# Kernel optimization log

Measured on AMD Instinct MI355X. Metric: run time of the kernel, lower is better.

The kernel has to match this reference:

```python
import jax, jax.numpy as jnp
import numpy as np

N_NODES = 200000
DEG = 16
T = 3


def _w(key, shape, scale=0.05):
    return (jax.random.normal(key, shape, dtype=jnp.float32) * scale)


def setup_inputs() -> dict:
    key = jax.random.key(0)
    ks = jax.random.split(key, 24)
    inp = {
        'h': jax.random.normal(ks[0], (N_NODES, 70), dtype=jnp.float32),
        'edge_feats': jax.random.normal(ks[1], (N_NODES, DEG, 6), dtype=jnp.float32),
        'nbr_idx': jax.random.randint(ks[2], (N_NODES, DEG), 0, N_NODES, dtype=jnp.int32),
        # V: Linear(70,70) (shared across all T rounds, since ModuleList([m]*T) aliases)
        'Vw': _w(ks[3], (70, 70)), 'Vb': _w(ks[4], (70,)),
        # E: Linear(6,6)
        'Ew': _w(ks[5], (6, 6)), 'Eb': _w(ks[6], (6,)),
        # U: Linear(146,70) (shared across rounds)
        'Uw': _w(ks[7], (146, 70)), 'Ub': _w(ks[8], (70,)),
        # R: Linear(140,128)
        'Rw': _w(ks[9], (140, 128)), 'Rb': _w(ks[10], (128,)),
        # shared_hidden1: 128->128, shared_hidden2: 128->100
        'S1w': _w(ks[11], (128, 128)), 'S1b': _w(ks[12], (128,)),
        'S2w': _w(ks[13], (128, 100)), 'S2b': _w(ks[14], (100,)),
        # task head (n_tasks=1): hidden 100->100, output 100->1
        'Hw': _w(ks[15], (100, 100)), 'Hb': _w(ks[16], (100,)),
        'Ow': _w(ks[17], (100, 1)), 'Ob': _w(ks[18], (1,)),
    }
    return inp


def reference(h, edge_feats, nbr_idx, Vw, Vb, Ew, Eb, Uw, Ub, Rw, Rb,
              S1w, S1b, S2w, S2b, Hw, Hb, Ow, Ob):
    # Message passing: per neighbor slot j (sequential state update, as the
    # original updates h[v] in place per neighbor), applied to all nodes at once.
    xs = (jnp.transpose(nbr_idx), jnp.swapaxes(edge_feats, 0, 1))  # [DEG,N], [DEG,N,6]

    def step(hc, x):
        idx, e = x
        m_w = hc[idx] @ Vw + Vb                 # gather neighbor states, V(h[w])
        m_e = e @ Ew + Eb                       # E(e_vw)
        hc = jax.nn.relu(jnp.concatenate([hc, m_w, m_e], axis=1) @ Uw + Ub)
        return hc, None

    for _ in range(T):  # U/V are shared across rounds (ModuleList aliasing)
        h, _ = jax.lax.scan(step, h, xs)

    # Readout: h2 aliases h in the original torch code, so cat([h, h]) (dim 140)
    fm = jnp.sum(jax.nn.relu(jnp.concatenate([h, h], axis=1) @ Rw + Rb), axis=0)  # [128]
    a = jax.nn.relu(fm @ S1w + S1b)   # ReLU(ReLU(.)) == ReLU(.)
    b = a @ S2w + S2b                 # no activation before hidden layer
    c = jax.nn.relu(b @ Hw + Hb)
    out = c @ Ow + Ob                 # [1]
    return out[None, :]               # [n_tasks=1, 1]
```

## Files before the change

### kernel.cpp

```cpp
#include <hip/hip_runtime.h>
#include <hip/hip_bf16.h>


#define NNODES 200000
#define DEG 16

typedef __attribute__((ext_vector_type(8))) short short8;
typedef __attribute__((ext_vector_type(4))) float f32x4;

__device__ __forceinline__ unsigned short f2bf(float f) {
    unsigned u = __float_as_uint(f);
    unsigned r = 0x7FFFu + ((u >> 16) & 1u);
    return (unsigned short)((u + r) >> 16);
}

__device__ __forceinline__ int kmap(int k) {
    if (k < 70) return k;
    if (k >= 96 && k < 166) return k - 26;
    if (k >= 192 && k < 198) return k - 52;
    return -1;
}

__global__ void prepA_kernel(const float* __restrict__ Vw, const float* __restrict__ Vb,
                             const float* __restrict__ Ew, const float* __restrict__ Eb,
                             const float* __restrict__ Uw, const float* __restrict__ Ub,
                             const float* __restrict__ Rw,
                             float* __restrict__ Bstep, float* __restrict__ bias80,
                             unsigned short* __restrict__ Rcg) {
    const int b = blockIdx.x, t = threadIdx.x;
    if (b < 70) {
        if (t < 70) {
            Bstep[b * 70 + t] = Uw[b * 70 + t];
            float s = 0.f;
            for (int c2 = 0; c2 < 70; ++c2) s += Vw[b * 70 + c2] * Uw[(70 + c2) * 70 + t];
            Bstep[(70 + b) * 70 + t] = s;
        }
    } else if (b == 70) {
        for (int i = t; i < 6 * 70; i += 256) {
            const int c = i / 70, n = i % 70;
            float s = 0.f;
            for (int c2 = 0; c2 < 6; ++c2) s += Ew[c * 6 + c2] * Uw[(140 + c2) * 70 + n];
            Bstep[(140 + c) * 70 + n] = s;
        }
    } else if (b == 71) {
        if (t < 80) {
            float s = 0.f;
            if (t < 70) {
                s = Ub[t];
                for (int c2 = 0; c2 < 70; ++c2) s += Vb[c2] * Uw[(70 + c2) * 70 + t];
                for (int c2 = 0; c2 < 6; ++c2) s += Eb[c2] * Uw[(140 + c2) * 70 + t];
            }
            bias80[t] = s;
        }
    } else {
        const int f = b - 72;
        const int nt = f & 7, kt = f >> 3;
        for (int e = t; e < 512; e += 256) {
            const int l = e >> 3, j = e & 7;
            const int col = nt * 16 + (l & 15);
            const int k = kt * 32 + (l >> 4) * 8 + j;
            const float v = (k < 70) ? (Rw[k * 128 + col] + Rw[(70 + k) * 128 + col]) : 0.f;
            Rcg[f * 512 + e] = f2bf(v);
        }
    }
}

__global__ void prepB_kernel(const float* __restrict__ Bstep, unsigned short* __restrict__ Btg) {
    const int f = blockIdx.x, t = threadIdx.x;
    const int nt = f % 5, kt = f / 5;
    for (int e = t; e < 512; e += 256) {
        const int l = e >> 3, j = e & 7;
        const int col = nt * 16 + (l & 15);
        const int k = kt * 32 + (l >> 4) * 8 + j;
        const int kr = kmap(k);
        const float v = (col < 70 && kr >= 0) ? Bstep[kr * 70 + col] : 0.f;
        Btg[f * 512 + e] = f2bf(v);
    }
}

__global__ void conv_h_kernel(const float* __restrict__ h0, unsigned short* __restrict__ hb) {
    const long total = (long)NNODES * 36;
    for (long i = (long)blockIdx.x * blockDim.x + threadIdx.x; i < total;
         i += (long)gridDim.x * blockDim.x) {
        const long node = i / 36;
        const int kp = (int)(i % 36);
        unsigned v = 0u;
        if (kp < 35) {
            const float* p = h0 + node * 70 + kp * 2;
            v = (unsigned)f2bf(p[0]) | ((unsigned)f2bf(p[1]) << 16);
        }
        ((unsigned*)(hb + node * 72))[kp] = v;
    }
}

__global__ void conv_e_kernel(const float* __restrict__ e, unsigned short* __restrict__ eb) {
    const long total = (long)NNODES * DEG * 4;
    for (long i = (long)blockIdx.x * blockDim.x + threadIdx.x; i < total;
         i += (long)gridDim.x * blockDim.x) {
        const long row = i / 4;
        const int c = (int)(i % 4);
        unsigned v = 0u;
        if (c < 3) {
            const float* p = e + row * 6 + c * 2;
            v = (unsigned)f2bf(p[0]) | ((unsigned)f2bf(p[1]) << 16);
        }
        ((unsigned*)(eb + row * 8))[c] = v;
    }
}

__global__ __launch_bounds__(512, 4) void step_kernel(
    const unsigned short* __restrict__ hin, const unsigned short* __restrict__ edgeb,
    const int* __restrict__ nbr, const unsigned short* __restrict__ Btg,
    const float* __restrict__ bias80, unsigned short* __restrict__ hout, const int j) {
    __shared__ __align__(16) unsigned short Btb[35 * 512];
    __shared__ float bias_s[80];
    const int tid = threadIdx.x;
    const long node0 = (long)blockIdx.x * 128;

    {
        const uint4* src = (const uint4*)Btg;
        uint4* dst = (uint4*)Btb;
        for (int i = tid; i < 2240; i += 512) dst[i] = src[i];
    }
    if (tid < 80) bias_s[tid] = bias80[tid];

    const int w = tid >> 6, l = tid & 63;
    const int lm = l & 15, lhi = l >> 4, lk = lhi * 8;
    const int lofs = l * 8;
    const long anode = node0 + w * 16 + lm;
    const long nl = anode < NNODES ? anode : (NNODES - 1);
    const int g = nbr[nl * DEG + j];

    short8 a[7];
    {
        const unsigned short* hr = hin + nl * 72;
        a[0] = *(const short8*)(hr + lk);
        a[1] = *(const short8*)(hr + 32 + lk);
        a[2] = *(const short8*)(hr + 64 + lk);
        const unsigned short* gr = hin + (long)g * 72;
        a[3] = *(const short8*)(gr + lk);
        a[4] = *(const short8*)(gr + 32 + lk);
        a[5] = *(const short8*)(gr + 64 + lk);
        a[6] = *(const short8*)(edgeb + (nl * DEG + j) * 8 + lk);
    }
    __syncthreads();

    f32x4 acc[5] = {{0.f, 0.f, 0.f, 0.f}, {0.f, 0.f, 0.f, 0.f}, {0.f, 0.f, 0.f, 0.f},
                    {0.f, 0.f, 0.f, 0.f}, {0.f, 0.f, 0.f, 0.f}};
#pragma unroll
    for (int kt = 0; kt < 7; ++kt) {
#pragma unroll
        for (int nt = 0; nt < 5; ++nt) {
            const short8 b = *(const short8*)&Btb[(kt * 5 + nt) * 512 + lofs];
            acc[nt] = __builtin_amdgcn_mfma_f32_16x16x32_bf16(a[kt], b, acc[nt], 0, 0, 0);
        }
    }

#pragma unroll
    for (int nt = 0; nt < 5; ++nt) {
        const int col = nt * 16 + lm;
        if (col < 70) {
            const float bias = bias_s[col];
#pragma unroll
            for (int r = 0; r < 4; ++r) {
                const long dnode = node0 + w * 16 + lhi * 4 + r;
                if (dnode < NNODES)
                    hout[dnode * 72 + col] = f2bf(fmaxf(acc[nt][r] + bias, 0.f));
            }
        }
    }
}

__global__ __launch_bounds__(512, 4) void readout_kernel(
    const unsigned short* __restrict__ hb, const unsigned short* __restrict__ Rcg,
    const float* __restrict__ Rb, float* __restrict__ fm) {
    __shared__ __align__(16) unsigned short Rs[24 * 512];
    __shared__ float Rb_s[128];
    __shared__ float red[8][128];
    const int tid = threadIdx.x;
    const long node0 = (long)blockIdx.x * 128;

    {
        const uint4* src = (const uint4*)Rcg;
        uint4* dst = (uint4*)Rs;
        for (int i = tid; i < 1536; i += 512) dst[i] = src[i];
    }
    if (tid < 128) Rb_s[tid] = Rb[tid];

    const int w = tid >> 6, l = tid & 63;
    const int lm = l & 15, lhi = l >> 4, lk = lhi * 8;
    const int lofs = l * 8;
    const long anode = node0 + w * 16 + lm;
    const long nl = anode < NNODES ? anode : (NNODES - 1);
    short8 a[3];
    {
        const unsigned short* hr = hb + nl * 72;
        a[0] = *(const short8*)(hr + lk);
        a[1] = *(const short8*)(hr + 32 + lk);
        a[2] = *(const short8*)(hr + 64 + lk);
    }
    __syncthreads();

    f32x4 acc[8] = {{0.f, 0.f, 0.f, 0.f}, {0.f, 0.f, 0.f, 0.f}, {0.f, 0.f, 0.f, 0.f},
                    {0.f, 0.f, 0.f, 0.f}, {0.f, 0.f, 0.f, 0.f}, {0.f, 0.f, 0.f, 0.f},
                    {0.f, 0.f, 0.f, 0.f}, {0.f, 0.f, 0.f, 0.f}};
#pragma unroll
    for (int kt = 0; kt < 3; ++kt) {
#pragma unroll
        for (int nt = 0; nt < 8; ++nt) {
            const short8 b = *(const short8*)&Rs[(kt * 8 + nt) * 512 + lofs];
            acc[nt] = __builtin_amdgcn_mfma_f32_16x16x32_bf16(a[kt], b, acc[nt], 0, 0, 0);
        }
    }
#pragma unroll
    for (int nt = 0; nt < 8; ++nt) {
        const int col = nt * 16 + lm;
        const float bias = Rb_s[col];
        float s = 0.f;
#pragma unroll
        for (int r = 0; r < 4; ++r) {
            const long dnode = node0 + w * 16 + lhi * 4 + r;
            if (dnode < NNODES) s += fmaxf(acc[nt][r] + bias, 0.f);
        }
        s += __shfl_xor(s, 16);
        s += __shfl_xor(s, 32);
        if (l < 16) red[w][col] = s;
    }
    __syncthreads();
    if (tid < 128) {
        float s = 0.f;
#pragma unroll
        for (int r = 0; r < 8; ++r) s += red[r][tid];
        atomicAdd(&fm[tid], s);
    }
}

__global__ void mlp_kernel(const float* __restrict__ fm,
                           const float* __restrict__ S1w, const float* __restrict__ S1b,
                           const float* __restrict__ S2w, const float* __restrict__ S2b,
                           const float* __restrict__ Hw, const float* __restrict__ Hb,
                           const float* __restrict__ Ow, const float* __restrict__ Ob,
                           float* __restrict__ out) {
    __shared__ float fms[128], a_s[128], b_s[100], c_s[100];
    const int t = threadIdx.x;
    fms[t] = fm[t];
    __syncthreads();
    {
        float s = S1b[t];
        for (int c = 0; c < 128; ++c) s += fms[c] * S1w[c * 128 + t];
        a_s[t] = fmaxf(s, 0.f);
    }
    __syncthreads();
    if (t < 100) {
        float s = S2b[t];
        for (int c = 0; c < 128; ++c) s += a_s[c] * S2w[c * 100 + t];
        b_s[t] = s;
    }
    __syncthreads();
    if (t < 100) {
        float s = Hb[t];
        for (int c = 0; c < 100; ++c) s += b_s[c] * Hw[c * 100 + t];
        c_s[t] = fmaxf(s, 0.f);
    }
    __syncthreads();
    if (t == 0) {
        float s = Ob[0];
        for (int c = 0; c < 100; ++c) s += c_s[c] * Ow[c];
        out[0] = s;
    }
}

extern "C" void kernel_launch(void* const* d_in, const int* in_sizes, int n_in,
                              void* d_out, int out_size, void* d_ws, size_t ws_size,
                              hipStream_t stream) {
    const float* h0   = (const float*)d_in[0];
    const float* edge = (const float*)d_in[1];
    const int*   nbr  = (const int*)d_in[2];
    const float* Vw = (const float*)d_in[3];
    const float* Vb = (const float*)d_in[4];
    const float* Ew = (const float*)d_in[5];
    const float* Eb = (const float*)d_in[6];
    const float* Uw = (const float*)d_in[7];
    const float* Ub = (const float*)d_in[8];
    const float* Rw = (const float*)d_in[9];
    const float* Rb = (const float*)d_in[10];
    const float* S1w = (const float*)d_in[11];
    const float* S1b = (const float*)d_in[12];
    const float* S2w = (const float*)d_in[13];
    const float* S2b = (const float*)d_in[14];
    const float* Hw = (const float*)d_in[15];
    const float* Hb = (const float*)d_in[16];
    const float* Ow = (const float*)d_in[17];
    const float* Ob = (const float*)d_in[18];
    float* out = (float*)d_out;

    char* ws = (char*)d_ws;
    unsigned short* hA    = (unsigned short*)(ws);
    unsigned short* hB    = (unsigned short*)(ws + 28801024);
    unsigned short* edgeb = (unsigned short*)(ws + 57602048);
    unsigned short* Btg   = (unsigned short*)(ws + 108803072);
    unsigned short* Rcg   = (unsigned short*)(ws + 108838912);
    float* bias80 = (float*)(ws + 108863488);
    float* fm     = (float*)(ws + 108863808);
    float* Bstep  = (float*)(ws + 108864320);

    conv_h_kernel<<<2048, 256, 0, stream>>>(h0, hA);
    conv_e_kernel<<<2048, 256, 0, stream>>>(edge, edgeb);
    prepA_kernel<<<96, 256, 0, stream>>>(Vw, Vb, Ew, Eb, Uw, Ub, Rw, Bstep, bias80, Rcg);
    prepB_kernel<<<35, 256, 0, stream>>>(Bstep, Btg);
    hipMemsetAsync(fm, 0, 128 * sizeof(float), stream);

    const int nblk = (NNODES + 127) / 128;
    const unsigned short* cur = hA;
    for (int s = 0; s < 48; ++s) {
        unsigned short* o = (s & 1) ? hA : hB;
        step_kernel<<<nblk, 512, 0, stream>>>(cur, edgeb, nbr, Btg, bias80, o, s & 15);
        cur = o;
    }
    readout_kernel<<<nblk, 512, 0, stream>>>(cur, Rcg, Rb, fm);
    mlp_kernel<<<1, 128, 0, stream>>>(fm, S1w, S1b, S2w, S2b, Hw, Hb, Ow, Ob, out);
}
```

Measured before the change: 1.665 ms.

## Make step kernel persistent with double-buffered A loads across node groups

The step kernel now launches 512 blocks instead of one per 128 nodes. Each wave handles up to four 16-node groups, strided by 4096 waves, and prefetches the next group's h, neighbor and edge rows into a second register buffer while it runs MFMAs on the current one. The goal is to load the bf16 weight tile into LDS once per block instead of once per 128 nodes, and to hide gather latency behind compute. The cost is more register pressure from two A buffers and fewer waves to cover latency; tail groups are guarded by validity flags.

```diff
diff --git a/kernel.cpp b/kernel.cpp
--- a/kernel.cpp
+++ b/kernel.cpp
@@ -4,6 +4,8 @@
 
 #define NNODES 200000
 #define DEG 16
+#define NGRP 12500
+#define NWAVES 4096
 
 typedef __attribute__((ext_vector_type(8))) short short8;
 typedef __attribute__((ext_vector_type(4))) float f32x4;
@@ -56,9 +58,9 @@
         const int f = b - 72;
         const int nt = f & 7, kt = f >> 3;
         for (int e = t; e < 512; e += 256) {
-            const int l = e >> 3, j = e & 7;
+            const int l = e >> 3, jj = e & 7;
             const int col = nt * 16 + (l & 15);
-            const int k = kt * 32 + (l >> 4) * 8 + j;
+            const int k = kt * 32 + (l >> 4) * 8 + jj;
             const float v = (k < 70) ? (Rw[k * 128 + col] + Rw[(70 + k) * 128 + col]) : 0.f;
             Rcg[f * 512 + e] = f2bf(v);
         }
@@ -69,9 +71,9 @@
     const int f = blockIdx.x, t = threadIdx.x;
     const int nt = f % 5, kt = f / 5;
     for (int e = t; e < 512; e += 256) {
-        const int l = e >> 3, j = e & 7;
+        const int l = e >> 3, jj = e & 7;
         const int col = nt * 16 + (l & 15);
-        const int k = kt * 32 + (l >> 4) * 8 + j;
+        const int k = kt * 32 + (l >> 4) * 8 + jj;
         const int kr = kmap(k);
         const float v = (col < 70 && kr >= 0) ? Bstep[kr * 70 + col] : 0.f;
         Btg[f * 512 + e] = f2bf(v);
@@ -115,7 +117,6 @@
     __shared__ __align__(16) unsigned short Btb[35 * 512];
     __shared__ float bias_s[80];
     const int tid = threadIdx.x;
-    const long node0 = (long)blockIdx.x * 128;
 
     {
         const uint4* src = (const uint4*)Btg;
@@ -127,13 +128,10 @@
     const int w = tid >> 6, l = tid & 63;
     const int lm = l & 15, lhi = l >> 4, lk = lhi * 8;
     const int lofs = l * 8;
-    const long anode = node0 + w * 16 + lm;
-    const long nl = anode < NNODES ? anode : (NNODES - 1);
-    const int g = nbr[nl * DEG + j];
-
-    short8 a[7];
-    {
-        const unsigned short* hr = hin + nl * 72;
+    const int gw = blockIdx.x * 8 + w;
+
+    auto loadA = [&](short8* a, long row, int g) {
+        const unsigned short* hr = hin + row * 72;
         a[0] = *(const short8*)(hr + lk);
         a[1] = *(const short8*)(hr + 32 + lk);
         a[2] = *(const short8*)(hr + 64 + lk);
@@ -141,34 +139,62 @@
         a[3] = *(const short8*)(gr + lk);
         a[4] = *(const short8*)(gr + 32 + lk);
         a[5] = *(const short8*)(gr + 64 + lk);
-        a[6] = *(const short8*)(edgeb + (nl * DEG + j) * 8 + lk);
-    }
-    __syncthreads();
-
-    f32x4 acc[5] = {{0.f, 0.f, 0.f, 0.f}, {0.f, 0.f, 0.f, 0.f}, {0.f, 0.f, 0.f, 0.f},
-                    {0.f, 0.f, 0.f, 0.f}, {0.f, 0.f, 0.f, 0.f}};
-#pragma unroll
-    for (int kt = 0; kt < 7; ++kt) {
+        a[6] = *(const short8*)(edgeb + (row * DEG + j) * 8 + lk);
+    };
+
+    auto doGroup = [&](const short8* a, long grp) {
+        f32x4 acc[5] = {{0.f, 0.f, 0.f, 0.f}, {0.f, 0.f, 0.f, 0.f}, {0.f, 0.f, 0.f, 0.f},
+                        {0.f, 0.f, 0.f, 0.f}, {0.f, 0.f, 0.f, 0.f}};
+#pragma unroll
+        for (int kt = 0; kt < 7; ++kt) {
+#pragma unroll
+            for (int nt = 0; nt < 5; ++nt) {
+                const short8 b = *(const short8*)&Btb[(kt * 5 + nt) * 512 + lofs];
+                acc[nt] = __builtin_amdgcn_mfma_f32_16x16x32_bf16(a[kt], b, acc[nt], 0, 0, 0);
+            }
+        }
 #pragma unroll
         for (int nt = 0; nt < 5; ++nt) {
-            const short8 b = *(const short8*)&Btb[(kt * 5 + nt) * 512 + lofs];
-            acc[nt] = __builtin_amdgcn_mfma_f32_16x16x32_bf16(a[kt], b, acc[nt], 0, 0, 0);
-        }
-    }
-
-#pragma unroll
-    for (int nt = 0; nt < 5; ++nt) {
-        const int col = nt * 16 + lm;
-        if (col < 70) {
-            const float bias = bias_s[col];
-#pragma unroll
-            for (int r = 0; r < 4; ++r) {
-                const long dnode = node0 + w * 16 + lhi * 4 + r;
-                if (dnode < NNODES)
-                    hout[dnode * 72 + col] = f2bf(fmaxf(acc[nt][r] + bias, 0.f));
+            const int col = nt * 16 + lm;
+            if (col < 70) {
+                const float bias = bias_s[col];
+#pragma unroll
+                for (int r = 0; r < 4; ++r) {
+                    const long node = grp * 16 + lhi * 4 + r;
+                    hout[node * 72 + col] = f2bf(fmaxf(acc[nt][r] + bias, 0.f));
+                }
             }
         }
-    }
+    };
+
+    const long r0 = (long)gw * 16 + lm;
+    const int g0 = nbr[r0 * DEG + j];
+    short8 A0[7], A1[7];
+    loadA(A0, r0, g0);
+    const long r1 = r0 + (long)NWAVES * 16;
+    const int g1 = nbr[r1 * DEG + j];
+    __syncthreads();
+
+    loadA(A1, r1, g1);
+    const int grp2 = gw + 2 * NWAVES;
+    const bool v2 = grp2 < NGRP;
+    const long r2 = r1 + (long)NWAVES * 16;
+    int g2 = 0;
+    if (v2) g2 = nbr[r2 * DEG + j];
+    doGroup(A0, gw);
+
+    if (v2) loadA(A0, r2, g2);
+    const int grp3 = gw + 3 * NWAVES;
+    const bool v3 = grp3 < NGRP;
+    const long r3 = r2 + (long)NWAVES * 16;
+    int g3 = 0;
+    if (v3) g3 = nbr[r3 * DEG + j];
+    doGroup(A1, gw + NWAVES);
+
+    if (v3) loadA(A1, r3, g3);
+    if (v2) doGroup(A0, grp2);
+
+    if (v3) doGroup(A1, grp3);
 }
 
 __global__ __launch_bounds__(512, 4) void readout_kernel(
@@ -310,13 +336,12 @@
     prepB_kernel<<<35, 256, 0, stream>>>(Bstep, Btg);
     hipMemsetAsync(fm, 0, 128 * sizeof(float), stream);
 
-    const int nblk = (NNODES + 127) / 128;
     const unsigned short* cur = hA;
     for (int s = 0; s < 48; ++s) {
         unsigned short* o = (s & 1) ? hA : hB;
-        step_kernel<<<nblk, 512, 0, stream>>>(cur, edgeb, nbr, Btg, bias80, o, s & 15);
+        step_kernel<<<512, 512, 0, stream>>>(cur, edgeb, nbr, Btg, bias80, o, s & 15);
         cur = o;
     }
-    readout_kernel<<<nblk, 512, 0, stream>>>(cur, Rcg, Rb, fm);
+    readout_kernel<<<(NNODES + 127) / 128, 512, 0, stream>>>(cur, Rcg, Rb, fm);
     mlp_kernel<<<1, 128, 0, stream>>>(fm, S1w, S1b, S2w, S2b, Hw, Hb, Ow, Ob, out);
 }
```

Measured after the change: 1.704 ms. +2.4%, slower.
